# Performance work log

Measured on AMD Instinct MI355X. Metric: run time of the kernel, lower is better.

The kernel has to match this reference:

```python
import jax, jax.numpy as jnp
import numpy as np
from jax import lax

# pywt db4 reconstruction low-pass (scaling) coefficients
_REC_LO = np.array([
    0.23037781330885523, 0.7148465705525415, 0.6308807679295904,
    -0.02798376941698385, -0.18703481171888114, 0.030841381835986965,
    0.032883011666982945, -0.010597401784997278], dtype=np.float64)
_DEC_LO = _REC_LO[::-1].copy()                       # pywt dec_lo = reversed rec_lo
_DEC_HI = (_REC_LO * ((-1.0) ** (np.arange(8) + 1)))  # pywt qmf: dec_hi[k] = (-1)^(k+1) rec_lo[k]
FLEN = 8
LEVEL = 4


def _dwt_level(x):
    """One pywt dwt level, mode='symmetric'. x: [N, n] -> (cA, cD) each [N, floor((n+7)/2)]."""
    # half-sample symmetric extension by FLEN-1 on each side, then drop the first
    # sample so a stride-2 VALID conv lands on pywt's odd-indexed outputs.
    ext = jnp.pad(x, ((0, 0), (FLEN - 1, FLEN - 1)), mode='symmetric')[:, 1:]
    # pywt performs true convolution with dec filters -> flip kernels for XLA correlation
    k = jnp.stack([_DEC_LO[::-1], _DEC_HI[::-1]]).astype(x.dtype)[:, None, :]  # [2,1,8]
    y = lax.conv_general_dilated(ext[:, None, :], k, window_strides=(2,),
                                 padding='VALID',
                                 dimension_numbers=('NCH', 'OIH', 'NCH'))  # [N,2,out]
    return y[:, 0], y[:, 1]


def setup_inputs() -> dict:
    key = jax.random.key(0)
    x = jax.random.normal(key, (64, 32, 8192), dtype=jnp.float32)
    return {"x": x}


def reference(x) -> jnp.ndarray:
    """Batched pywt.wavedec(x, 'db4', mode='symmetric', level=4), coeffs concatenated.
    x: [B, C, L] -> [B, C, wavelet_len] with order [cA4, cD4, cD3, cD2, cD1]."""
    B, C, L = x.shape
    a = x.reshape(B * C, L)
    details = []
    for _ in range(LEVEL):
        a, d = _dwt_level(a)
        details.append(d)
    coeffs = jnp.concatenate([a] + details[::-1], axis=-1)  # [B*C, total]
    return coeffs.reshape(B, C, -1)
```

## Files before the change

kernel.cpp:

```cpp
#include <hip/hip_runtime.h>

#define NT 256

constexpr int LPAD = 8;
constexpr int L0 = 8192;
constexpr int N1 = 4099;
constexpr int N2 = 2053;
constexpr int N3 = 1030;
constexpr int N4 = 518;
constexpr int ROW_OUT = N4 + N4 + N3 + N2 + N1;

constexpr float GLO[8] = {
    0.23037781330885523f,  0.7148465705525415f,   0.6308807679295904f,
   -0.02798376941698385f, -0.18703481171888114f,  0.030841381835986965f,
    0.032883011666982945f, -0.010597401784997278f };
constexpr float GHI[8] = {
   -0.010597401784997278f, -0.032883011666982945f, 0.030841381835986965f,
    0.18703481171888114f,  -0.02798376941698385f,  -0.6308807679295904f,
    0.7148465705525415f,   -0.23037781330885523f };

__device__ __forceinline__ void dwt_level_lds(const float* __restrict__ in, int nout,
                                              float* __restrict__ lo_out,
                                              float* __restrict__ hi_out, int tid)
{
    for (int i = tid; i < nout; i += NT) {
        const float* p = in + 2 * i + 2;
        float lo = 0.f, hi = 0.f;
#pragma unroll
        for (int j = 0; j < 8; ++j) {
            float v = p[j];
            lo = fmaf(GLO[j], v, lo);
            hi = fmaf(GHI[j], v, hi);
        }
        lo_out[i] = lo;
        hi_out[i] = hi;
    }
}

__global__ __launch_bounds__(NT) void wavedec4_db4(const float* __restrict__ x,
                                                   float* __restrict__ out)
{
    __shared__ float bufA[LPAD + L0 + 8];
    __shared__ float bufB[LPAD + N1 + 8];
    const int tid = threadIdx.x;
    const size_t row = blockIdx.x;
    const float* __restrict__ xr = x + row * (size_t)L0;
    float* __restrict__ outr = out + row * (size_t)ROW_OUT;

    const float4* x4 = (const float4*)xr;
    float4* a4 = (float4*)(bufA + LPAD);
    for (int i = tid; i < L0 / 4; i += NT) a4[i] = x4[i];
    if (tid < 7) {
        bufA[LPAD - 1 - tid] = xr[tid];
        bufA[LPAD + L0 + tid] = xr[L0 - 1 - tid];
    }
    __syncthreads();

    dwt_level_lds(bufA, N1, bufB + LPAD, outr + (N4 + N4 + N3 + N2), tid);
    __syncthreads();
    if (tid < 7) {
        bufB[LPAD - 1 - tid] = bufB[LPAD + tid];
        bufB[LPAD + N1 + tid] = bufB[LPAD + N1 - 1 - tid];
    }
    __syncthreads();

    dwt_level_lds(bufB, N2, bufA + LPAD, outr + (N4 + N4 + N3), tid);
    __syncthreads();
    if (tid < 7) {
        bufA[LPAD - 1 - tid] = bufA[LPAD + tid];
        bufA[LPAD + N2 + tid] = bufA[LPAD + N2 - 1 - tid];
    }
    __syncthreads();

    dwt_level_lds(bufA, N3, bufB + LPAD, outr + (N4 + N4), tid);
    __syncthreads();
    if (tid < 7) {
        bufB[LPAD - 1 - tid] = bufB[LPAD + tid];
        bufB[LPAD + N3 + tid] = bufB[LPAD + N3 - 1 - tid];
    }
    __syncthreads();

    dwt_level_lds(bufB, N4, outr, outr + N4, tid);
}

extern "C" void kernel_launch(void* const* d_in, const int* in_sizes, int n_in,
                              void* d_out, int out_size, void* d_ws, size_t ws_size,
                              hipStream_t stream) {
    const float* x = (const float*)d_in[0];
    float* out = (float*)d_out;
    const int rows = in_sizes[0] / L0;
    wavedec4_db4<<<dim3(rows), dim3(NT), 0, stream>>>(x, out);
}
```

Baseline: 116.6 us.

## Compute level 1 from global memory, register-block 4 outputs, swizzle LDS

Measured after the change: 126.6 us. +8.6%, slower.

```diff
diff --git a/kernel.cpp b/kernel.cpp
--- a/kernel.cpp
+++ b/kernel.cpp
@@ -2,13 +2,16 @@
 
 #define NT 256
 
-constexpr int LPAD = 8;
 constexpr int L0 = 8192;
 constexpr int N1 = 4099;
 constexpr int N2 = 2053;
 constexpr int N3 = 1030;
 constexpr int N4 = 518;
 constexpr int ROW_OUT = N4 + N4 + N3 + N2 + N1;
+constexpr int LPAD = 8;
+
+constexpr int B1_SLOTS = 1032;
+constexpr int B2_SLOTS = 520;
 
 constexpr float GLO[8] = {
     0.23037781330885523f,  0.7148465705525415f,   0.6308807679295904f,
@@ -19,68 +22,134 @@
     0.18703481171888114f,  -0.02798376941698385f,  -0.6308807679295904f,
     0.7148465705525415f,   -0.23037781330885523f };
 
-__device__ __forceinline__ void dwt_level_lds(const float* __restrict__ in, int nout,
-                                              float* __restrict__ lo_out,
-                                              float* __restrict__ hi_out, int tid)
+__device__ __forceinline__ int swz_slot(int s) { return s ^ ((s >> 3) & 7); }
+__device__ __forceinline__ int swzf(int f) { return (swz_slot(f >> 2) << 2) | (f & 3); }
+
+__device__ __forceinline__ void conv4(const float* __restrict__ w,
+                                      float* __restrict__ lo,
+                                      float* __restrict__ hi)
 {
-    for (int i = tid; i < nout; i += NT) {
-        const float* p = in + 2 * i + 2;
-        float lo = 0.f, hi = 0.f;
+#pragma unroll
+    for (int m = 0; m < 4; ++m) {
+        float l = 0.f, h = 0.f;
 #pragma unroll
         for (int j = 0; j < 8; ++j) {
-            float v = p[j];
-            lo = fmaf(GLO[j], v, lo);
-            hi = fmaf(GHI[j], v, hi);
+            float v = w[2 * m + 2 + j];
+            l = fmaf(GLO[j], v, l);
+            h = fmaf(GHI[j], v, h);
         }
-        lo_out[i] = lo;
-        hi_out[i] = hi;
+        lo[m] = l;
+        hi[m] = h;
+    }
+}
+
+__device__ __forceinline__ void store_lo_lds(float* __restrict__ bout, int nout,
+                                             int t, const float* __restrict__ lo)
+{
+    const int i0 = 4 * t;
+    if (i0 + 4 <= nout) {
+        *(float4*)(bout + 4 * swz_slot(t + 2)) = make_float4(lo[0], lo[1], lo[2], lo[3]);
+    } else {
+#pragma unroll
+        for (int m = 0; m < 4; ++m)
+            if (i0 + m < nout) bout[swzf(LPAD + i0 + m)] = lo[m];
+    }
+    if (t < 2) {
+#pragma unroll
+        for (int m = 0; m < 4; ++m) {
+            int i = i0 + m;
+            if (i < 7) bout[swzf(LPAD - 1 - i)] = lo[m];
+        }
+    }
+    if (i0 + 3 >= nout - 7) {
+#pragma unroll
+        for (int m = 0; m < 4; ++m) {
+            int i = i0 + m;
+            if (i < nout && i >= nout - 7) bout[swzf(LPAD + 2 * nout - 1 - i)] = lo[m];
+        }
+    }
+}
+
+__device__ __forceinline__ void level1(const float* __restrict__ xr,
+                                       float* __restrict__ bout,
+                                       float* __restrict__ hi_g, int tid)
+{
+    constexpr int ntask = (N1 + 3) >> 2;
+    for (int t = tid; t < ntask; t += NT) {
+        float w[16];
+        if (t >= 1 && t < (L0 / 8)) {
+            const float4* p = (const float4*)(xr + 8 * t - 8);
+            float4 r0 = p[0], r1 = p[1], r2 = p[2], r3 = p[3];
+            w[0] = r0.x;  w[1] = r0.y;  w[2] = r0.z;  w[3] = r0.w;
+            w[4] = r1.x;  w[5] = r1.y;  w[6] = r1.z;  w[7] = r1.w;
+            w[8] = r2.x;  w[9] = r2.y;  w[10] = r2.z; w[11] = r2.w;
+            w[12] = r3.x; w[13] = r3.y; w[14] = r3.z; w[15] = r3.w;
+        } else {
+#pragma unroll
+            for (int j = 0; j < 16; ++j) {
+                int q = 8 * t - 8 + j;
+                q = (q < 0) ? (-1 - q) : q;
+                q = (q >= L0) ? (2 * L0 - 1 - q) : q;
+                w[j] = xr[q];
+            }
+        }
+        float lo[4], hi[4];
+        conv4(w, lo, hi);
+        store_lo_lds(bout, N1, t, lo);
+        const int i0 = 4 * t;
+#pragma unroll
+        for (int m = 0; m < 4; ++m)
+            if (i0 + m < N1) hi_g[i0 + m] = hi[m];
+    }
+}
+
+template<bool LAST>
+__device__ __forceinline__ void level_lds(const float* __restrict__ bin, int nout,
+                                          float* __restrict__ bout,
+                                          float* __restrict__ lo_g,
+                                          float* __restrict__ hi_g, int tid)
+{
+    const int ntask = (nout + 3) >> 2;
+    for (int t = tid; t < ntask; t += NT) {
+        float4 r0 = *(const float4*)(bin + 4 * swz_slot(2 * t + 0));
+        float4 r1 = *(const float4*)(bin + 4 * swz_slot(2 * t + 1));
+        float4 r2 = *(const float4*)(bin + 4 * swz_slot(2 * t + 2));
+        float4 r3 = *(const float4*)(bin + 4 * swz_slot(2 * t + 3));
+        float w[16] = { r0.x, r0.y, r0.z, r0.w, r1.x, r1.y, r1.z, r1.w,
+                        r2.x, r2.y, r2.z, r2.w, r3.x, r3.y, r3.z, r3.w };
+        float lo[4], hi[4];
+        conv4(w, lo, hi);
+        const int i0 = 4 * t;
+        if (LAST) {
+#pragma unroll
+            for (int m = 0; m < 4; ++m)
+                if (i0 + m < nout) lo_g[i0 + m] = lo[m];
+        } else {
+            store_lo_lds(bout, nout, t, lo);
+        }
+#pragma unroll
+        for (int m = 0; m < 4; ++m)
+            if (i0 + m < nout) hi_g[i0 + m] = hi[m];
     }
 }
 
 __global__ __launch_bounds__(NT) void wavedec4_db4(const float* __restrict__ x,
                                                    float* __restrict__ out)
 {
-    __shared__ float bufA[LPAD + L0 + 8];
-    __shared__ float bufB[LPAD + N1 + 8];
+    __shared__ float B1[B1_SLOTS * 4];
+    __shared__ float B2[B2_SLOTS * 4];
     const int tid = threadIdx.x;
     const size_t row = blockIdx.x;
     const float* __restrict__ xr = x + row * (size_t)L0;
     float* __restrict__ outr = out + row * (size_t)ROW_OUT;
 
-    const float4* x4 = (const float4*)xr;
-    float4* a4 = (float4*)(bufA + LPAD);
-    for (int i = tid; i < L0 / 4; i += NT) a4[i] = x4[i];
-    if (tid < 7) {
-        bufA[LPAD - 1 - tid] = xr[tid];
-        bufA[LPAD + L0 + tid] = xr[L0 - 1 - tid];
-    }
+    level1(xr, B1, outr + (N4 + N4 + N3 + N2), tid);
     __syncthreads();
-
-    dwt_level_lds(bufA, N1, bufB + LPAD, outr + (N4 + N4 + N3 + N2), tid);
+    level_lds<false>(B1, N2, B2, nullptr, outr + (N4 + N4 + N3), tid);
     __syncthreads();
-    if (tid < 7) {
-        bufB[LPAD - 1 - tid] = bufB[LPAD + tid];
-        bufB[LPAD + N1 + tid] = bufB[LPAD + N1 - 1 - tid];
-    }
+    level_lds<false>(B2, N3, B1, nullptr, outr + (N4 + N4), tid);
     __syncthreads();
-
-    dwt_level_lds(bufB, N2, bufA + LPAD, outr + (N4 + N4 + N3), tid);
-    __syncthreads();
-    if (tid < 7) {
-        bufA[LPAD - 1 - tid] = bufA[LPAD + tid];
-        bufA[LPAD + N2 + tid] = bufA[LPAD + N2 - 1 - tid];
-    }
-    __syncthreads();
-
-    dwt_level_lds(bufA, N3, bufB + LPAD, outr + (N4 + N4), tid);
-    __syncthreads();
-    if (tid < 7) {
-        bufB[LPAD - 1 - tid] = bufB[LPAD + tid];
-        bufB[LPAD + N3 + tid] = bufB[LPAD + N3 - 1 - tid];
-    }
-    __syncthreads();
-
-    dwt_level_lds(bufB, N4, outr, outr + N4, tid);
+    level_lds<true>(B1, N4, nullptr, outr, outr + N4, tid);
 }
 
 extern "C" void kernel_launch(void* const* d_in, const int* in_sizes, int n_in,
```

## Keep per-thread wavelet windows in registers across levels with small LDS halos

Applied to the files above, without the earlier changes.

Result: no change. 116.4 us (-0.2%).

```diff
diff --git a/kernel.cpp b/kernel.cpp
--- a/kernel.cpp
+++ b/kernel.cpp
@@ -1,14 +1,20 @@
 #include <hip/hip_runtime.h>
 
-#define NT 256
-
-constexpr int LPAD = 8;
+#define NT 512
+
 constexpr int L0 = 8192;
 constexpr int N1 = 4099;
 constexpr int N2 = 2053;
 constexpr int N3 = 1030;
 constexpr int N4 = 518;
 constexpr int ROW_OUT = N4 + N4 + N3 + N2 + N1;
+constexpr int OFF_A4 = 0;
+constexpr int OFF_D4 = 518;
+constexpr int OFF_D3 = 1036;
+constexpr int OFF_D2 = 2066;
+constexpr int OFF_D1 = 4119;
+
+constexpr int HS = 520;
 
 constexpr float GLO[8] = {
     0.23037781330885523f,  0.7148465705525415f,   0.6308807679295904f,
@@ -19,68 +25,185 @@
     0.18703481171888114f,  -0.02798376941698385f,  -0.6308807679295904f,
     0.7148465705525415f,   -0.23037781330885523f };
 
-__device__ __forceinline__ void dwt_level_lds(const float* __restrict__ in, int nout,
-                                              float* __restrict__ lo_out,
-                                              float* __restrict__ hi_out, int tid)
+__global__ __launch_bounds__(NT, 8) void wavedec4_db4(const float* __restrict__ x,
+                                                      float* __restrict__ out)
 {
-    for (int i = tid; i < nout; i += NT) {
-        const float* p = in + 2 * i + 2;
-        float lo = 0.f, hi = 0.f;
-#pragma unroll
-        for (int j = 0; j < 8; ++j) {
-            float v = p[j];
-            lo = fmaf(GLO[j], v, lo);
-            hi = fmaf(GHI[j], v, hi);
-        }
-        lo_out[i] = lo;
-        hi_out[i] = hi;
-    }
-}
-
-__global__ __launch_bounds__(NT) void wavedec4_db4(const float* __restrict__ x,
-                                                   float* __restrict__ out)
-{
-    __shared__ float bufA[LPAD + L0 + 8];
-    __shared__ float bufB[LPAD + N1 + 8];
-    const int tid = threadIdx.x;
-    const size_t row = blockIdx.x;
-    const float* __restrict__ xr = x + row * (size_t)L0;
-    float* __restrict__ outr = out + row * (size_t)ROW_OUT;
-
-    const float4* x4 = (const float4*)xr;
-    float4* a4 = (float4*)(bufA + LPAD);
-    for (int i = tid; i < L0 / 4; i += NT) a4[i] = x4[i];
-    if (tid < 7) {
-        bufA[LPAD - 1 - tid] = xr[tid];
-        bufA[LPAD + L0 + tid] = xr[L0 - 1 - tid];
+    __shared__ float hA[8 * HS];
+    __shared__ float hB[4 * HS];
+    const int t = threadIdx.x;
+    const float* __restrict__ xr = x + blockIdx.x * (size_t)L0;
+    float* __restrict__ outr = out + blockIdx.x * (size_t)ROW_OUT;
+
+    float xw[24];
+    if (t > 0) {
+        const float4* p = (const float4*)(xr + 16 * t - 8);
+        float4 v0 = p[0], v1 = p[1], v2 = p[2], v3 = p[3], v4 = p[4], v5 = p[5];
+        xw[0] = v0.x;  xw[1] = v0.y;  xw[2] = v0.z;  xw[3] = v0.w;
+        xw[4] = v1.x;  xw[5] = v1.y;  xw[6] = v1.z;  xw[7] = v1.w;
+        xw[8] = v2.x;  xw[9] = v2.y;  xw[10] = v2.z; xw[11] = v2.w;
+        xw[12] = v3.x; xw[13] = v3.y; xw[14] = v3.z; xw[15] = v3.w;
+        xw[16] = v4.x; xw[17] = v4.y; xw[18] = v4.z; xw[19] = v4.w;
+        xw[20] = v5.x; xw[21] = v5.y; xw[22] = v5.z; xw[23] = v5.w;
+    } else {
+        const float4* p = (const float4*)xr;
+        float4 v0 = p[0], v1 = p[1], v2 = p[2], v3 = p[3];
+        xw[8] = v0.x;  xw[9] = v0.y;  xw[10] = v0.z; xw[11] = v0.w;
+        xw[12] = v1.x; xw[13] = v1.y; xw[14] = v1.z; xw[15] = v1.w;
+        xw[16] = v2.x; xw[17] = v2.y; xw[18] = v2.z; xw[19] = v2.w;
+        xw[20] = v3.x; xw[21] = v3.y; xw[22] = v3.z; xw[23] = v3.w;
+#pragma unroll
+        for (int k = 0; k < 8; ++k) xw[k] = xw[15 - k];
+    }
+
+    float lo1[8];
+#pragma unroll
+    for (int m = 0; m < 8; ++m) {
+        float l = 0.f, h = 0.f;
+#pragma unroll
+        for (int j = 0; j < 8; ++j) {
+            float v = xw[2 * m + 2 + j];
+            l = fmaf(GLO[j], v, l);
+            h = fmaf(GHI[j], v, h);
+        }
+        lo1[m] = l;
+        outr[OFF_D1 + 8 * t + m] = h;
+        hA[m * HS + t] = l;
+    }
+    if (t == 8) {
+        float xt[6];
+#pragma unroll
+        for (int k = 0; k < 6; ++k) xt[k] = xr[8186 + k];
+#pragma unroll
+        for (int e = 0; e < 3; ++e) {
+            const int i = 4096 + e;
+            float l = 0.f, h = 0.f;
+#pragma unroll
+            for (int j = 0; j < 8; ++j) {
+                int q = 2 * i - 6 + j;
+                int idx = ((q <= 8191) ? q : (16383 - q)) - 8186;
+                float v = xt[idx];
+                l = fmaf(GLO[j], v, l);
+                h = fmaf(GHI[j], v, h);
+            }
+            outr[OFF_D1 + i] = h;
+            hA[(i & 7) * HS + (i >> 3)] = l;
+        }
     }
     __syncthreads();
 
-    dwt_level_lds(bufA, N1, bufB + LPAD, outr + (N4 + N4 + N3 + N2), tid);
+    float w2[14];
+#pragma unroll
+    for (int k = 0; k < 6; ++k) {
+        int g = 8 * t - 6 + k;
+        if (g < 0) g = -1 - g;
+        w2[k] = hA[(g & 7) * HS + (g >> 3)];
+    }
+#pragma unroll
+    for (int m = 0; m < 8; ++m) w2[6 + m] = lo1[m];
+    float lo2[4];
+#pragma unroll
+    for (int m = 0; m < 4; ++m) {
+        float l = 0.f, h = 0.f;
+#pragma unroll
+        for (int j = 0; j < 8; ++j) {
+            float v = w2[2 * m + j];
+            l = fmaf(GLO[j], v, l);
+            h = fmaf(GHI[j], v, h);
+        }
+        lo2[m] = l;
+        outr[OFF_D2 + 4 * t + m] = h;
+        hB[m * HS + t] = l;
+    }
+    if (t < 5) {
+        const int jj = 2048 + t;
+        float l = 0.f, h = 0.f;
+#pragma unroll
+        for (int j = 0; j < 8; ++j) {
+            int g = 2 * jj - 6 + j;
+            if (g > 4098) g = 8197 - g;
+            float v = hA[(g & 7) * HS + (g >> 3)];
+            l = fmaf(GLO[j], v, l);
+            h = fmaf(GHI[j], v, h);
+        }
+        outr[OFF_D2 + jj] = h;
+        hB[(jj & 3) * HS + (jj >> 2)] = l;
+    }
     __syncthreads();
-    if (tid < 7) {
-        bufB[LPAD - 1 - tid] = bufB[LPAD + tid];
-        bufB[LPAD + N1 + tid] = bufB[LPAD + N1 - 1 - tid];
+
+    float w3[10];
+#pragma unroll
+    for (int k = 0; k < 6; ++k) {
+        int g = 4 * t - 6 + k;
+        if (g < 0) g = -1 - g;
+        w3[k] = hB[(g & 3) * HS + (g >> 2)];
+    }
+#pragma unroll
+    for (int m = 0; m < 4; ++m) w3[6 + m] = lo2[m];
+    float lo3[2];
+#pragma unroll
+    for (int m = 0; m < 2; ++m) {
+        float l = 0.f, h = 0.f;
+#pragma unroll
+        for (int j = 0; j < 8; ++j) {
+            float v = w3[2 * m + j];
+            l = fmaf(GLO[j], v, l);
+            h = fmaf(GHI[j], v, h);
+        }
+        lo3[m] = l;
+        outr[OFF_D3 + 2 * t + m] = h;
+        hA[m * HS + t] = l;
+    }
+    if (t < 6) {
+        const int jj = 1024 + t;
+        float l = 0.f, h = 0.f;
+#pragma unroll
+        for (int j = 0; j < 8; ++j) {
+            int g = 2 * jj - 6 + j;
+            if (g > 2052) g = 4105 - g;
+            float v = hB[(g & 3) * HS + (g >> 2)];
+            l = fmaf(GLO[j], v, l);
+            h = fmaf(GHI[j], v, h);
+        }
+        outr[OFF_D3 + jj] = h;
+        const int gg = jj;
+        hA[(gg & 1) * HS + (gg >> 1)] = l;
     }
     __syncthreads();
 
-    dwt_level_lds(bufB, N2, bufA + LPAD, outr + (N4 + N4 + N3), tid);
-    __syncthreads();
-    if (tid < 7) {
-        bufA[LPAD - 1 - tid] = bufA[LPAD + tid];
-        bufA[LPAD + N2 + tid] = bufA[LPAD + N2 - 1 - tid];
-    }
-    __syncthreads();
-
-    dwt_level_lds(bufA, N3, bufB + LPAD, outr + (N4 + N4), tid);
-    __syncthreads();
-    if (tid < 7) {
-        bufB[LPAD - 1 - tid] = bufB[LPAD + tid];
-        bufB[LPAD + N3 + tid] = bufB[LPAD + N3 - 1 - tid];
-    }
-    __syncthreads();
-
-    dwt_level_lds(bufB, N4, outr, outr + N4, tid);
+    float w4[8];
+#pragma unroll
+    for (int k = 0; k < 6; ++k) {
+        int g = 2 * t - 6 + k;
+        if (g < 0) g = -1 - g;
+        w4[k] = hA[(g & 1) * HS + (g >> 1)];
+    }
+    w4[6] = lo3[0];
+    w4[7] = lo3[1];
+    {
+        float l = 0.f, h = 0.f;
+#pragma unroll
+        for (int j = 0; j < 8; ++j) {
+            float v = w4[j];
+            l = fmaf(GLO[j], v, l);
+            h = fmaf(GHI[j], v, h);
+        }
+        outr[OFF_A4 + t] = l;
+        outr[OFF_D4 + t] = h;
+    }
+    if (t < 6) {
+        const int jj = 512 + t;
+        float l = 0.f, h = 0.f;
+#pragma unroll
+        for (int j = 0; j < 8; ++j) {
+            int g = 2 * jj - 6 + j;
+            if (g > 1029) g = 2059 - g;
+            float v = hA[(g & 1) * HS + (g >> 1)];
+            l = fmaf(GLO[j], v, l);
+            h = fmaf(GHI[j], v, h);
+        }
+        outr[OFF_A4 + jj] = l;
+        outr[OFF_D4 + jj] = h;
+    }
 }
 
 extern "C" void kernel_launch(void* const* d_in, const int* in_sizes, int n_in,
```

## Split each row into per-wavefront tiles with halo recompute, dropping block syncs

Applied to the files above, without the earlier changes.

Result: slower. 139.6 us (+19.7%).

```diff
diff --git a/kernel.cpp b/kernel.cpp
--- a/kernel.cpp
+++ b/kernel.cpp
@@ -2,13 +2,20 @@
 
 #define NT 256
 
-constexpr int LPAD = 8;
 constexpr int L0 = 8192;
 constexpr int N1 = 4099;
 constexpr int N2 = 2053;
 constexpr int N3 = 1030;
 constexpr int N4 = 518;
 constexpr int ROW_OUT = N4 + N4 + N3 + N2 + N1;
+constexpr int OFF_A4 = 0;
+constexpr int OFF_D4 = 518;
+constexpr int OFF_D3 = 1036;
+constexpr int OFF_D2 = 2066;
+constexpr int OFF_D1 = 4119;
+
+constexpr int S1 = 576, S2 = 320, S3 = 192;
+constexpr int SW = S1 + S2 + S3;
 
 constexpr float GLO[8] = {
     0.23037781330885523f,  0.7148465705525415f,   0.6308807679295904f,
@@ -19,68 +26,152 @@
     0.18703481171888114f,  -0.02798376941698385f,  -0.6308807679295904f,
     0.7148465705525415f,   -0.23037781330885523f };
 
-__device__ __forceinline__ void dwt_level_lds(const float* __restrict__ in, int nout,
-                                              float* __restrict__ lo_out,
-                                              float* __restrict__ hi_out, int tid)
+__device__ __forceinline__ void conv1(const float* __restrict__ w,
+                                      float& lo, float& hi)
 {
-    for (int i = tid; i < nout; i += NT) {
-        const float* p = in + 2 * i + 2;
-        float lo = 0.f, hi = 0.f;
+    float l = 0.f, h = 0.f;
 #pragma unroll
-        for (int j = 0; j < 8; ++j) {
-            float v = p[j];
-            lo = fmaf(GLO[j], v, lo);
-            hi = fmaf(GHI[j], v, hi);
-        }
-        lo_out[i] = lo;
-        hi_out[i] = hi;
+    for (int j = 0; j < 8; ++j) {
+        float v = w[j];
+        l = fmaf(GLO[j], v, l);
+        h = fmaf(GHI[j], v, h);
     }
+    lo = l; hi = h;
 }
 
-__global__ __launch_bounds__(NT) void wavedec4_db4(const float* __restrict__ x,
-                                                   float* __restrict__ out)
+__global__ __launch_bounds__(NT, 8) void wavedec4_db4(const float* __restrict__ x,
+                                                      float* __restrict__ out)
 {
-    __shared__ float bufA[LPAD + L0 + 8];
-    __shared__ float bufB[LPAD + N1 + 8];
+    __shared__ float lds[4 * SW];
     const int tid = threadIdx.x;
-    const size_t row = blockIdx.x;
-    const float* __restrict__ xr = x + row * (size_t)L0;
-    float* __restrict__ outr = out + row * (size_t)ROW_OUT;
+    const int widx = tid >> 6;
+    const int l = tid & 63;
+    const int gw = blockIdx.x * 4 + widx;
+    const int row = gw >> 3;
+    const int w = gw & 7;
 
-    const float4* x4 = (const float4*)xr;
-    float4* a4 = (float4*)(bufA + LPAD);
-    for (int i = tid; i < L0 / 4; i += NT) a4[i] = x4[i];
-    if (tid < 7) {
-        bufA[LPAD - 1 - tid] = xr[tid];
-        bufA[LPAD + L0 + tid] = xr[L0 - 1 - tid];
+    const float* __restrict__ xr = x + (size_t)row * L0;
+    float* __restrict__ outr = out + (size_t)row * ROW_OUT;
+    float* __restrict__ s1 = lds + widx * SW;
+    float* __restrict__ s2 = s1 + S1;
+    float* __restrict__ s3 = s2 + S2;
+
+    const int B1 = 512 * w - 48;
+    const int B2 = 256 * w - 18;
+    const int B3 = 128 * w - 6;
+    const int hi1 = (w == 7) ? N1 : 512 * w + 512;
+    const int hi2 = (w == 7) ? N2 : 256 * w + 256;
+    const int hi3 = (w == 7) ? N3 : 128 * w + 128;
+    const bool interior = (w != 0) && (w != 7);
+
+    float xw[24];
+    const int bl = 2 * B1 - 6 + 18 * l;
+    if (bl >= 0 && bl + 24 <= L0) {
+        const float2* p = (const float2*)(xr + bl);
+#pragma unroll
+        for (int k = 0; k < 12; ++k) { float2 v = p[k]; xw[2 * k] = v.x; xw[2 * k + 1] = v.y; }
+    } else {
+#pragma unroll
+        for (int k = 0; k < 24; ++k) {
+            int q = bl + k;
+            q = (q < 0) ? (-1 - q) : q;
+            q = (q >= L0) ? (2 * L0 - 1 - q) : q;
+            xw[k] = xr[q];
+        }
     }
-    __syncthreads();
+#pragma unroll
+    for (int m = 0; m < 9; ++m) {
+        float lo, hi;
+        conv1(xw + 2 * m, lo, hi);
+        s1[9 * l + m] = lo;
+        const int c = B1 + 9 * l + m;
+        if (c >= 512 * w && c < hi1) outr[OFF_D1 + c] = hi;
+    }
 
-    dwt_level_lds(bufA, N1, bufB + LPAD, outr + (N4 + N4 + N3 + N2), tid);
-    __syncthreads();
-    if (tid < 7) {
-        bufB[LPAD - 1 - tid] = bufB[LPAD + tid];
-        bufB[LPAD + N1 + tid] = bufB[LPAD + N1 - 1 - tid];
+    float wb[16];
+    if (interior) {
+        const float2* p = (const float2*)(s1 + 10 * l + 6);
+#pragma unroll
+        for (int k = 0; k < 8; ++k) { float2 v = p[k]; wb[2 * k] = v.x; wb[2 * k + 1] = v.y; }
+    } else {
+        const int g0 = 2 * B2 - 6 + 10 * l;
+#pragma unroll
+        for (int k = 0; k < 16; ++k) {
+            int g = g0 + k;
+            g = (g < 0) ? (-1 - g) : g;
+            g = (g >= N1) ? (2 * N1 - 1 - g) : g;
+            wb[k] = s1[g - B1];
+        }
     }
-    __syncthreads();
+#pragma unroll
+    for (int m = 0; m < 5; ++m) {
+        float lo, hi;
+        conv1(wb + 2 * m, lo, hi);
+        s2[5 * l + m] = lo;
+        const int c = B2 + 5 * l + m;
+        if (c >= 256 * w && c < hi2) outr[OFF_D2 + c] = hi;
+    }
 
-    dwt_level_lds(bufB, N2, bufA + LPAD, outr + (N4 + N4 + N3), tid);
-    __syncthreads();
-    if (tid < 7) {
-        bufA[LPAD - 1 - tid] = bufA[LPAD + tid];
-        bufA[LPAD + N2 + tid] = bufA[LPAD + N2 - 1 - tid];
+    float wc[12];
+    if (interior) {
+        const float2* p = (const float2*)(s2 + 6 * l);
+#pragma unroll
+        for (int k = 0; k < 6; ++k) { float2 v = p[k]; wc[2 * k] = v.x; wc[2 * k + 1] = v.y; }
+    } else {
+        const int g0 = 2 * B3 - 6 + 6 * l;
+#pragma unroll
+        for (int k = 0; k < 12; ++k) {
+            int g = g0 + k;
+            g = (g < 0) ? (-1 - g) : g;
+            g = (g >= N2) ? (2 * N2 - 1 - g) : g;
+            wc[k] = s2[g - B2];
+        }
     }
-    __syncthreads();
+#pragma unroll
+    for (int m = 0; m < 3; ++m) {
+        float lo, hi;
+        conv1(wc + 2 * m, lo, hi);
+        s3[3 * l + m] = lo;
+        const int c = B3 + 3 * l + m;
+        if (c >= 128 * w && c < hi3) outr[OFF_D3 + c] = hi;
+    }
 
-    dwt_level_lds(bufA, N3, bufB + LPAD, outr + (N4 + N4), tid);
-    __syncthreads();
-    if (tid < 7) {
-        bufB[LPAD - 1 - tid] = bufB[LPAD + tid];
-        bufB[LPAD + N3 + tid] = bufB[LPAD + N3 - 1 - tid];
+    float wd[8];
+    if (interior) {
+        const float2* p = (const float2*)(s3 + 2 * l);
+#pragma unroll
+        for (int k = 0; k < 4; ++k) { float2 v = p[k]; wd[2 * k] = v.x; wd[2 * k + 1] = v.y; }
+    } else {
+        const int g0 = 128 * w - 6 + 2 * l;
+#pragma unroll
+        for (int k = 0; k < 8; ++k) {
+            int g = g0 + k;
+            g = (g < 0) ? (-1 - g) : g;
+            g = (g >= N3) ? (2 * N3 - 1 - g) : g;
+            wd[k] = s3[g - B3];
+        }
     }
-    __syncthreads();
-
-    dwt_level_lds(bufB, N4, outr, outr + N4, tid);
+    {
+        float lo, hi;
+        conv1(wd, lo, hi);
+        const int c = 64 * w + l;
+        outr[OFF_A4 + c] = lo;
+        outr[OFF_D4 + c] = hi;
+    }
+    if (w == 7 && l < 6) {
+        float we[8];
+#pragma unroll
+        for (int k = 0; k < 8; ++k) {
+            int g = 1018 + 2 * l + k;
+            g = (g >= N3) ? (2 * N3 - 1 - g) : g;
+            we[k] = s3[g - B3];
+        }
+        float lo, hi;
+        conv1(we, lo, hi);
+        const int c = 512 + l;
+        outr[OFF_A4 + c] = lo;
+        outr[OFF_D4 + c] = hi;
+    }
 }
 
 extern "C" void kernel_launch(void* const* d_in, const int* in_sizes, int n_in,
@@ -89,5 +180,5 @@
     const float* x = (const float*)d_in[0];
     float* out = (float*)d_out;
     const int rows = in_sizes[0] / L0;
-    wavedec4_db4<<<dim3(rows), dim3(NT), 0, stream>>>(x, out);
+    wavedec4_db4<<<dim3(rows * 2), dim3(NT), 0, stream>>>(x, out);
 }
```
